# Performance work log

Hardware: AMD Instinct MI355X
Metric: run time of the kernel (lower is better)

The kernel has to match this reference:

```python
import jax, jax.numpy as jnp
import numpy as np

B, S, DIM = 4, 512, 2048
E, INTER = 32, 1024
G, TOPK_G, TOPK = 8, 4, 6
ROUTE_SCALE = 2.5
SHARED_INTER = 2 * INTER  # n_shared_experts * moe_inter_dim


def setup_inputs() -> dict:
    key = jax.random.key(0)
    ks = jax.random.split(key, 8)
    sd = 0.02
    return {
        "x": jax.random.normal(ks[0], (B, S, DIM), jnp.float32),
        "gate_w": jax.random.normal(ks[1], (E, DIM), jnp.float32) * sd,
        "w11": jax.random.normal(ks[2], (E, INTER, DIM), jnp.float32) * sd,  # gate proj (torch Linear weight [out,in])
        "w33": jax.random.normal(ks[3], (E, INTER, DIM), jnp.float32) * sd,  # up proj
        "w22": jax.random.normal(ks[4], (E, DIM, INTER), jnp.float32) * sd,  # down proj
        "sw1": jax.random.normal(ks[5], (SHARED_INTER, DIM), jnp.float32) * sd,
        "sw2": jax.random.normal(ks[6], (DIM, SHARED_INTER), jnp.float32) * sd,
        "sw3": jax.random.normal(ks[7], (SHARED_INTER, DIM), jnp.float32) * sd,
    }


def _gate(xf, gate_w):
    # sigmoid scores, group-limited greedy top-k (bias=None branch)
    scores = jax.nn.sigmoid(xf @ gate_w.T)                      # [T, E]
    gs = scores.reshape(-1, G, E // G)                          # [T, G, E/G]
    group_scores = gs.max(axis=-1)                              # amax since bias is None
    _, gidx = jax.lax.top_k(group_scores, TOPK_G)               # [T, TOPK_G]
    gmask = jnp.any(jnp.arange(G)[None, None, :] == gidx[:, :, None], axis=1)  # [T, G] keep-mask
    masked = jnp.where(gmask[:, :, None], gs, -jnp.inf).reshape(-1, E)
    _, idx = jax.lax.top_k(masked, TOPK)                        # [T, TOPK]
    w = jnp.take_along_axis(scores, idx, axis=1)                # gather from original (pre-mask) scores
    w = w / jnp.sum(w, axis=-1, keepdims=True) * ROUTE_SCALE    # sigmoid normalization + route_scale
    return w, idx


def reference(x, gate_w, w11, w33, w22, sw1, sw2, sw3):
    xf = x.reshape(-1, DIM)                                     # [T, D]
    T = xf.shape[0]
    w, idx = _gate(xf, gate_w)
    # dense combine weights: equals the gather->gmm->scatter*prob of the original
    c = jnp.zeros((T, E), xf.dtype).at[jnp.arange(T)[:, None], idx].add(w)  # [T, E]
    g = jnp.einsum('td,eid->tei', xf, w11)                      # fc1 (gate)
    u = jnp.einsum('td,eid->tei', xf, w33)                      # fc2 (up)
    act = jax.nn.silu(g) * u                                    # fused SiLU gating
    y = jnp.einsum('tei,te,edi->td', act, c, w22)               # down proj + weighted combine
    shared = (jax.nn.silu(xf @ sw1.T) * (xf @ sw3.T)) @ sw2.T   # shared experts MLP
    return (y + shared).reshape(x.shape)
```

## Files before the change

kernel.cpp:

```cpp
#include <hip/hip_runtime.h>
#include <hip/hip_bf16.h>

#define T_TOK  2048
#define DIMSZ  2048
#define NEXP   32
#define INTERS 1024
#define SINTER 2048
#define NTOPK  6

typedef __bf16 bf16x8 __attribute__((ext_vector_type(8)));
typedef float  f32x4  __attribute__((ext_vector_type(4)));
typedef unsigned short u16x8 __attribute__((ext_vector_type(8)));

__device__ __forceinline__ unsigned short f2b(float f) {
    __hip_bfloat16 h = __float2bfloat16(f);
    return __builtin_bit_cast(unsigned short, h);
}

__device__ __forceinline__ void gl_lds16(const unsigned short* g, unsigned short* l) {
    __builtin_amdgcn_global_load_lds(
        (const __attribute__((address_space(1))) void*)g,
        (__attribute__((address_space(3))) void*)l, 16, 0, 0);
}
__device__ __forceinline__ void gl_lds16f(const float* g, float* l) {
    __builtin_amdgcn_global_load_lds(
        (const __attribute__((address_space(1))) void*)g,
        (__attribute__((address_space(3))) void*)l, 16, 0, 0);
}

__device__ __forceinline__ bf16x8 cvt8(float4 lo, float4 hi) {
    u16x8 u;
    u[0] = f2b(lo.x); u[1] = f2b(lo.y); u[2] = f2b(lo.z); u[3] = f2b(lo.w);
    u[4] = f2b(hi.x); u[5] = f2b(hi.y); u[6] = f2b(hi.z); u[7] = f2b(hi.w);
    return __builtin_bit_cast(bf16x8, u);
}

__global__ void cvt_f2b(const float4* __restrict__ src, unsigned short* __restrict__ dst, int n8) {
    int stride = gridDim.x * blockDim.x;
    for (int i = blockIdx.x * blockDim.x + threadIdx.x; i < n8; i += stride) {
        float4 a = src[2 * (size_t)i];
        float4 b = src[2 * (size_t)i + 1];
        u16x8 o;
        o[0] = f2b(a.x); o[1] = f2b(a.y); o[2] = f2b(a.z); o[3] = f2b(a.w);
        o[4] = f2b(b.x); o[5] = f2b(b.y); o[6] = f2b(b.z); o[7] = f2b(b.w);
        *(u16x8*)&dst[(size_t)i * 8] = o;
    }
}

#define SCT 8
#define SCK 128
__global__ __launch_bounds__(256) void gate_scores_kernel(
    const float* __restrict__ x, const float* __restrict__ gw, float* __restrict__ scores)
{
    __shared__ float xs[SCT * SCK];
    __shared__ float gs[NEXP * (SCK + 1)];
    const int t0 = blockIdx.x * SCT;
    const int tid = threadIdx.x;
    const int tl = tid >> 5, e = tid & 31;
    float acc = 0.f;
    for (int k0 = 0; k0 < DIMSZ; k0 += SCK) {
        {
            int row = tid >> 5, d4 = tid & 31;
            *(float4*)&xs[row * SCK + d4 * 4] =
                *(const float4*)&x[(size_t)(t0 + row) * DIMSZ + k0 + d4 * 4];
        }
        #pragma unroll
        for (int i = 0; i < 4; ++i) {
            int lin = tid + i * 256;
            int row = lin >> 5, d4 = lin & 31;
            float4 v = *(const float4*)&gw[(size_t)row * DIMSZ + k0 + d4 * 4];
            float* dst = &gs[row * (SCK + 1) + d4 * 4];
            dst[0] = v.x; dst[1] = v.y; dst[2] = v.z; dst[3] = v.w;
        }
        __syncthreads();
        #pragma unroll 8
        for (int d = 0; d < SCK; ++d)
            acc += xs[tl * SCK + d] * gs[e * (SCK + 1) + d];
        __syncthreads();
    }
    scores[(size_t)(t0 + tl) * NEXP + e] = 1.f / (1.f + expf(-acc));
}

__global__ __launch_bounds__(256) void topk_kernel(
    const float* __restrict__ scores,
    int* __restrict__ counts, int* __restrict__ toklist, float* __restrict__ wgts)
{
    int t = blockIdx.x * 256 + threadIdx.x;
    if (t >= T_TOK) return;
    float sc[NEXP];
    #pragma unroll
    for (int e = 0; e < NEXP; ++e) sc[e] = scores[(size_t)t * NEXP + e];

    float gsc[8];
    #pragma unroll
    for (int g = 0; g < 8; ++g) {
        float m = sc[4 * g];
        #pragma unroll
        for (int j = 1; j < 4; ++j) m = fmaxf(m, sc[4 * g + j]);
        gsc[g] = m;
    }
    bool gsel[8] = {false, false, false, false, false, false, false, false};
    for (int it = 0; it < 4; ++it) {
        int bi = -1; float bv = -1e30f;
        #pragma unroll
        for (int g = 0; g < 8; ++g)
            if (!gsel[g] && gsc[g] > bv) { bv = gsc[g]; bi = g; }
        gsel[bi] = true;
    }
    bool esel[NEXP];
    #pragma unroll
    for (int e = 0; e < NEXP; ++e) esel[e] = false;
    int   idx[NTOPK];
    float w[NTOPK];
    float sum = 0.f;
    for (int it = 0; it < NTOPK; ++it) {
        int bi = -1; float bv = -1e30f;
        #pragma unroll
        for (int e = 0; e < NEXP; ++e) {
            if (!gsel[e >> 2] || esel[e]) continue;
            if (sc[e] > bv) { bv = sc[e]; bi = e; }
        }
        esel[bi] = true; idx[it] = bi; w[it] = bv; sum += bv;
    }
    float scale = 2.5f / sum;
    for (int k = 0; k < NTOPK; ++k) {
        int e = idx[k];
        int s = atomicAdd(&counts[e], 1);
        toklist[e * T_TOK + s] = (t << 3) | k;
        wgts[e * T_TOK + s]   = w[k] * scale;
    }
}

__device__ __forceinline__ void walk_experts(
    int ty, const int* __restrict__ counts, int& fe, int& fy, int& frb)
{
    int acc2 = 0, rb = 0;
    fe = -1; fy = 0; frb = 0;
    #pragma unroll
    for (int e2 = 0; e2 < NEXP; ++e2) {
        const int cnt = counts[e2];
        const int nt = (cnt + 127) >> 7;
        if (fe < 0 && ty < acc2 + nt) { fe = e2; fy = ty - acc2; frb = rb; }
        acc2 += nt; rb += cnt;
    }
}

__global__ __launch_bounds__(256, 3) void fc1_all(
    const unsigned short* __restrict__ A,
    const float* __restrict__ w11, const float* __restrict__ w33,
    const float* __restrict__ sw1, const float* __restrict__ sw3,
    unsigned short* __restrict__ h, unsigned short* __restrict__ hs,
    const int* __restrict__ counts, const int* __restrict__ toklist)
{
    constexpr int BK = 64, K = DIMSZ, NT = K / BK;
    __shared__ unsigned short As[128 * 64];
    __shared__ float B1s[64 * 64];
    __shared__ float B2s[64 * 64];

    const int tid = threadIdx.x;
    bool SH; int e, m0, n0, hbase = 0;
    {
        const int wgid = blockIdx.x;
        if (wgid < 512) {
            SH = true; e = NEXP; m0 = (wgid >> 5) * 128; n0 = (wgid & 31) * 64;
        } else {
            const int rid = wgid - 512;
            const int xt = rid & 15, ty = rid >> 4;
            int fe, fy, frb;
            walk_experts(ty, counts, fe, fy, frb);
            SH = false; e = fe; m0 = fy * 128; n0 = xt * 64; hbase = frb;
        }
    }
    if (!SH && e < 0) return;
    const int N = SH ? SINTER : INTERS;
    const int M = SH ? T_TOK : counts[e];

    const size_t eoff = SH ? 0 : (size_t)e * INTERS * DIMSZ;
    const float* B1 = (SH ? sw1 : w11) + eoff + (size_t)n0 * K;
    const float* B2 = (SH ? sw3 : w33) + eoff + (size_t)n0 * K;
    unsigned short* Hout = SH ? hs : h;

    const int wave = tid >> 6;
    const int lane = tid & 63;
    const int wm = (wave >> 1) * 64;
    const int wn = (wave & 1) * 32;
    const int lm = lane & 15;
    const int quad = lane >> 4;

    const unsigned short* aP[4];
    {
        const int l8 = lane >> 3;
        const int sg = (lane & 7) ^ l8;
        #pragma unroll
        for (int i = 0; i < 4; ++i) {
            const int row = (wave * 4 + i) * 8 + l8;
            const int gr = m0 + row;
            int ar;
            if (SH) ar = gr;
            else ar = (gr < M) ? (toklist[e * T_TOK + gr] >> 3) : 0;
            aP[i] = A + (size_t)ar * K + sg * 8;
        }
    }
    int offB[4];
    {
        #pragma unroll
        for (int i = 0; i < 4; ++i) {
            const int c = wave * 4 + i;
            const int row = 4 * c + (lane >> 4);
            const int g = (lane & 15) ^ (row & 7);
            offB[i] = row * K + g * 4;
        }
    }

    f32x4 acc1[4][2] = {};
    f32x4 acc2v[4][2] = {};

    for (int t = 0; t < NT; ++t) {
        const int k0 = t * BK;
        #pragma unroll
        for (int i = 0; i < 4; ++i)
            gl_lds16(aP[i] + k0, &As[(wave * 4 + i) * 512]);
        #pragma unroll
        for (int i = 0; i < 4; ++i) {
            gl_lds16f(B1 + offB[i] + k0, &B1s[(wave * 4 + i) * 256]);
            gl_lds16f(B2 + offB[i] + k0, &B2s[(wave * 4 + i) * 256]);
        }
        __syncthreads();

        #pragma unroll
        for (int kh = 0; kh < 2; ++kh) {
            const int soffA = (((kh << 2) | quad) ^ (lm & 7)) << 3;
            const int j0 = ((kh << 2) | quad) << 1;
            const int s0 = j0 ^ (lm & 7);
            const int s1 = (j0 | 1) ^ (lm & 7);
            bf16x8 af[4], bf1[2], bf2[2];
            #pragma unroll
            for (int ti = 0; ti < 4; ++ti)
                af[ti] = *(const bf16x8*)&As[(wm + ti * 16 + lm) * 64 + soffA];
            #pragma unroll
            for (int tj = 0; tj < 2; ++tj) {
                const int rB = (wn + tj * 16 + lm) * 64;
                bf1[tj] = cvt8(*(const float4*)&B1s[rB + s0 * 4],
                               *(const float4*)&B1s[rB + s1 * 4]);
                bf2[tj] = cvt8(*(const float4*)&B2s[rB + s0 * 4],
                               *(const float4*)&B2s[rB + s1 * 4]);
            }
            #pragma unroll
            for (int ti = 0; ti < 4; ++ti)
                #pragma unroll
                for (int tj = 0; tj < 2; ++tj) {
                    acc1[ti][tj] = __builtin_amdgcn_mfma_f32_16x16x32_bf16(
                        af[ti], bf1[tj], acc1[ti][tj], 0, 0, 0);
                    acc2v[ti][tj] = __builtin_amdgcn_mfma_f32_16x16x32_bf16(
                        af[ti], bf2[tj], acc2v[ti][tj], 0, 0, 0);
                }
        }
        __syncthreads();
    }

    #pragma unroll
    for (int ti = 0; ti < 4; ++ti) {
        #pragma unroll
        for (int r = 0; r < 4; ++r) {
            const int lrow = wm + ti * 16 + quad * 4 + r;
            const int grow = m0 + lrow;
            if (!SH && grow >= M) continue;
            const int cr = SH ? grow : (hbase + grow);
            #pragma unroll
            for (int tj = 0; tj < 2; ++tj) {
                int nn = n0 + wn + tj * 16 + lm;
                float g = acc1[ti][tj][r];
                float u = acc2v[ti][tj][r];
                float hv = g / (1.f + expf(-g)) * u;
                Hout[(size_t)cr * N + nn] = f2b(hv);
            }
        }
    }
}

__global__ __launch_bounds__(256, 3) void fc2_all(
    const unsigned short* __restrict__ h, const unsigned short* __restrict__ hs,
    const float* __restrict__ w22, const float* __restrict__ sw2,
    float* __restrict__ out,
    const int* __restrict__ counts, const int* __restrict__ toklist,
    const float* __restrict__ wgts)
{
    constexpr int BK = 32;
    __shared__ unsigned short As[128 * 32];
    __shared__ float Bs[128 * 32];

    const int tid = threadIdx.x;
    bool SH; int e, m0, n0, hbase = 0;
    {
        const int wgid = blockIdx.x;
        if (wgid < 256) {
            SH = true; e = NEXP; m0 = (wgid >> 4) * 128; n0 = (wgid & 15) * 128;
        } else {
            const int rid = wgid - 256;
            const int xt = rid & 15, ty = rid >> 4;
            int fe, fy, frb;
            walk_experts(ty, counts, fe, fy, frb);
            SH = false; e = fe; m0 = fy * 128; n0 = xt * 128; hbase = frb;
        }
    }
    if (!SH && e < 0) return;
    const int K = SH ? SINTER : INTERS;
    const int NT = K / BK;
    const int M = SH ? T_TOK : counts[e];
    if (m0 >= M) return;

    const unsigned short* Asrc = SH ? hs : h;
    const float* B = (SH ? sw2 : (w22 + (size_t)e * DIMSZ * INTERS)) + (size_t)n0 * K;

    const int wave = tid >> 6;
    const int lane = tid & 63;
    const int wm = (wave >> 1) * 64;
    const int wn = (wave & 1) * 64;
    const int lm = lane & 15;
    const int quad = lane >> 4;

    const unsigned short* aP[2];
    {
        const int gs = (lane & 3) ^ ((lane >> 3) & 3);
        #pragma unroll
        for (int i = 0; i < 2; ++i) {
            const int row = (wave * 2 + i) * 16 + (lane >> 2);
            const int gr = m0 + row;
            int ar;
            if (SH) ar = gr;
            else ar = hbase + ((gr < M) ? gr : 0);
            aP[i] = Asrc + (size_t)ar * K + gs * 8;
        }
    }
    int offB[4];
    {
        const int gs = (lane & 7) ^ (lane >> 3);
        #pragma unroll
        for (int i = 0; i < 4; ++i) {
            const int row = (wave * 4 + i) * 8 + (lane >> 3);
            offB[i] = row * K + gs * 4;
        }
    }

    f32x4 acc[4][4] = {};

    const int ga = quad ^ ((lm >> 1) & 3);
    const int s0 = (quad << 1) ^ (lm & 7);
    const int s1 = s0 ^ 1;

    for (int t = 0; t < NT; ++t) {
        const int k0 = t * BK;
        #pragma unroll
        for (int i = 0; i < 2; ++i)
            gl_lds16(aP[i] + k0, &As[(wave * 2 + i) * 512]);
        #pragma unroll
        for (int i = 0; i < 4; ++i)
            gl_lds16f(B + offB[i] + k0, &Bs[(wave * 4 + i) * 256]);
        __syncthreads();

        bf16x8 af[4], bfr[4];
        #pragma unroll
        for (int ti = 0; ti < 4; ++ti)
            af[ti] = *(const bf16x8*)&As[(wm + ti * 16 + lm) * 32 + ga * 8];
        #pragma unroll
        for (int tj = 0; tj < 4; ++tj) {
            const int rB = (wn + tj * 16 + lm) * 32;
            bfr[tj] = cvt8(*(const float4*)&Bs[rB + s0 * 4],
                           *(const float4*)&Bs[rB + s1 * 4]);
        }
        #pragma unroll
        for (int ti = 0; ti < 4; ++ti)
            #pragma unroll
            for (int tj = 0; tj < 4; ++tj)
                acc[ti][tj] = __builtin_amdgcn_mfma_f32_16x16x32_bf16(
                    af[ti], bfr[tj], acc[ti][tj], 0, 0, 0);

        __syncthreads();
    }

    #pragma unroll
    for (int ti = 0; ti < 4; ++ti) {
        #pragma unroll
        for (int r = 0; r < 4; ++r) {
            const int lrow = wm + ti * 16 + quad * 4 + r;
            const int grow = m0 + lrow;
            int cr; float cw;
            if (SH) { cr = grow; cw = 1.f; }
            else {
                if (grow >= M) continue;
                int ent = toklist[e * T_TOK + grow];
                cr = ent >> 3;
                cw = wgts[e * T_TOK + grow];
            }
            #pragma unroll
            for (int tj = 0; tj < 4; ++tj) {
                int nn = n0 + wn + tj * 16 + lm;
                atomicAdd(&out[(size_t)cr * DIMSZ + nn], acc[ti][tj][r] * cw);
            }
        }
    }
}

extern "C" void kernel_launch(void* const* d_in, const int* in_sizes, int n_in,
                              void* d_out, int out_size, void* d_ws, size_t ws_size,
                              hipStream_t stream)
{
    const float* x   = (const float*)d_in[0];
    const float* gw  = (const float*)d_in[1];
    const float* w11 = (const float*)d_in[2];
    const float* w33 = (const float*)d_in[3];
    const float* w22 = (const float*)d_in[4];
    const float* sw1 = (const float*)d_in[5];
    const float* sw2 = (const float*)d_in[6];
    const float* sw3 = (const float*)d_in[7];
    float* out = (float*)d_out;

    char* ws = (char*)d_ws;
    size_t off = 0;
    auto alloc = [&](size_t b) { void* p = ws + off; off = (off + b + 255) & ~(size_t)255; return p; };
    int*            counts  = (int*)alloc(NEXP * 4);
    int*            toklist = (int*)alloc((size_t)NEXP * T_TOK * 4);
    float*          wgts    = (float*)alloc((size_t)NEXP * T_TOK * 4);
    float*          scores  = (float*)alloc((size_t)T_TOK * NEXP * 4);
    unsigned short* xb      = (unsigned short*)alloc((size_t)T_TOK * DIMSZ * 2);
    unsigned short* h       = (unsigned short*)alloc(((size_t)T_TOK * NTOPK + 128) * INTERS * 2);
    unsigned short* hs      = (unsigned short*)alloc((size_t)T_TOK * SINTER * 2);

    hipMemsetAsync(counts, 0, NEXP * 4, stream);
    hipMemsetAsync(out, 0, out_size, stream);

    cvt_f2b<<<1024, 256, 0, stream>>>((const float4*)x, xb, T_TOK * DIMSZ / 8);

    gate_scores_kernel<<<T_TOK / SCT, 256, 0, stream>>>(x, gw, scores);
    topk_kernel<<<(T_TOK + 255) / 256, 256, 0, stream>>>(scores, counts, toklist, wgts);

    fc1_all<<<512 + 2048, 256, 0, stream>>>(
        xb, w11, w33, sw1, sw3, h, hs, counts, toklist);

    fc2_all<<<256 + 2048, 256, 0, stream>>>(
        h, hs, w22, sw2, out, counts, toklist, wgts);
}
```

Baseline: 1.040 ms.

## Double-buffer LDS tiles in fc1 and fc2 to overlap loads with MFMA

```diff
diff --git a/kernel.cpp b/kernel.cpp
--- a/kernel.cpp
+++ b/kernel.cpp
@@ -152,10 +152,10 @@
     unsigned short* __restrict__ h, unsigned short* __restrict__ hs,
     const int* __restrict__ counts, const int* __restrict__ toklist)
 {
-    constexpr int BK = 64, K = DIMSZ, NT = K / BK;
-    __shared__ unsigned short As[128 * 64];
-    __shared__ float B1s[64 * 64];
-    __shared__ float B2s[64 * 64];
+    constexpr int BK = 32, K = DIMSZ, NT = K / BK;
+    __shared__ unsigned short As[2][128 * 32];
+    __shared__ float B1s[2][64 * 32];
+    __shared__ float B2s[2][64 * 32];
 
     const int tid = threadIdx.x;
     bool SH; int e, m0, n0, hbase = 0;
@@ -187,75 +187,80 @@
     const int lm = lane & 15;
     const int quad = lane >> 4;
 
-    const unsigned short* aP[4];
-    {
-        const int l8 = lane >> 3;
-        const int sg = (lane & 7) ^ l8;
-        #pragma unroll
-        for (int i = 0; i < 4; ++i) {
-            const int row = (wave * 4 + i) * 8 + l8;
+    const unsigned short* aP[2];
+    {
+        const int gs = (lane & 3) ^ ((lane >> 3) & 3);
+        #pragma unroll
+        for (int i = 0; i < 2; ++i) {
+            const int row = (wave * 2 + i) * 16 + (lane >> 2);
             const int gr = m0 + row;
             int ar;
             if (SH) ar = gr;
             else ar = (gr < M) ? (toklist[e * T_TOK + gr] >> 3) : 0;
-            aP[i] = A + (size_t)ar * K + sg * 8;
-        }
-    }
-    int offB[4];
-    {
-        #pragma unroll
-        for (int i = 0; i < 4; ++i) {
-            const int c = wave * 4 + i;
-            const int row = 4 * c + (lane >> 4);
-            const int g = (lane & 15) ^ (row & 7);
-            offB[i] = row * K + g * 4;
+            aP[i] = A + (size_t)ar * K + gs * 8;
+        }
+    }
+    int offB[2];
+    {
+        const int gs = (lane & 7) ^ (lane >> 3);
+        #pragma unroll
+        for (int i = 0; i < 2; ++i) {
+            const int row = (wave * 2 + i) * 8 + (lane >> 3);
+            offB[i] = row * K + gs * 4;
         }
     }
 
     f32x4 acc1[4][2] = {};
     f32x4 acc2v[4][2] = {};
 
+    const int ga = quad ^ ((lm >> 1) & 3);
+    const int s0 = (quad << 1) ^ (lm & 7);
+    const int s1 = s0 ^ 1;
+
+    #pragma unroll
+    for (int i = 0; i < 2; ++i) {
+        gl_lds16(aP[i], &As[0][(wave * 2 + i) * 512]);
+        gl_lds16f(B1 + offB[i], &B1s[0][(wave * 2 + i) * 256]);
+        gl_lds16f(B2 + offB[i], &B2s[0][(wave * 2 + i) * 256]);
+    }
+    __syncthreads();
+
+    int buf = 0;
     for (int t = 0; t < NT; ++t) {
-        const int k0 = t * BK;
-        #pragma unroll
-        for (int i = 0; i < 4; ++i)
-            gl_lds16(aP[i] + k0, &As[(wave * 4 + i) * 512]);
-        #pragma unroll
-        for (int i = 0; i < 4; ++i) {
-            gl_lds16f(B1 + offB[i] + k0, &B1s[(wave * 4 + i) * 256]);
-            gl_lds16f(B2 + offB[i] + k0, &B2s[(wave * 4 + i) * 256]);
-        }
+        if (t + 1 < NT) {
+            const int kn = (t + 1) * BK;
+            #pragma unroll
+            for (int i = 0; i < 2; ++i) {
+                gl_lds16(aP[i] + kn, &As[buf ^ 1][(wave * 2 + i) * 512]);
+                gl_lds16f(B1 + offB[i] + kn, &B1s[buf ^ 1][(wave * 2 + i) * 256]);
+                gl_lds16f(B2 + offB[i] + kn, &B2s[buf ^ 1][(wave * 2 + i) * 256]);
+            }
+        }
+
+        bf16x8 af[4], bf1[2], bf2[2];
+        #pragma unroll
+        for (int ti = 0; ti < 4; ++ti)
+            af[ti] = *(const bf16x8*)&As[buf][(wm + ti * 16 + lm) * 32 + ga * 8];
+        #pragma unroll
+        for (int tj = 0; tj < 2; ++tj) {
+            const int rB = (wn + tj * 16 + lm) * 32;
+            bf1[tj] = cvt8(*(const float4*)&B1s[buf][rB + s0 * 4],
+                           *(const float4*)&B1s[buf][rB + s1 * 4]);
+            bf2[tj] = cvt8(*(const float4*)&B2s[buf][rB + s0 * 4],
+                           *(const float4*)&B2s[buf][rB + s1 * 4]);
+        }
+        #pragma unroll
+        for (int ti = 0; ti < 4; ++ti)
+            #pragma unroll
+            for (int tj = 0; tj < 2; ++tj) {
+                acc1[ti][tj] = __builtin_amdgcn_mfma_f32_16x16x32_bf16(
+                    af[ti], bf1[tj], acc1[ti][tj], 0, 0, 0);
+                acc2v[ti][tj] = __builtin_amdgcn_mfma_f32_16x16x32_bf16(
+                    af[ti], bf2[tj], acc2v[ti][tj], 0, 0, 0);
+            }
+
         __syncthreads();
-
-        #pragma unroll
-        for (int kh = 0; kh < 2; ++kh) {
-            const int soffA = (((kh << 2) | quad) ^ (lm & 7)) << 3;
-            const int j0 = ((kh << 2) | quad) << 1;
-            const int s0 = j0 ^ (lm & 7);
-            const int s1 = (j0 | 1) ^ (lm & 7);
-            bf16x8 af[4], bf1[2], bf2[2];
-            #pragma unroll
-            for (int ti = 0; ti < 4; ++ti)
-                af[ti] = *(const bf16x8*)&As[(wm + ti * 16 + lm) * 64 + soffA];
-            #pragma unroll
-            for (int tj = 0; tj < 2; ++tj) {
-                const int rB = (wn + tj * 16 + lm) * 64;
-                bf1[tj] = cvt8(*(const float4*)&B1s[rB + s0 * 4],
-                               *(const float4*)&B1s[rB + s1 * 4]);
-                bf2[tj] = cvt8(*(const float4*)&B2s[rB + s0 * 4],
-                               *(const float4*)&B2s[rB + s1 * 4]);
-            }
-            #pragma unroll
-            for (int ti = 0; ti < 4; ++ti)
-                #pragma unroll
-                for (int tj = 0; tj < 2; ++tj) {
-                    acc1[ti][tj] = __builtin_amdgcn_mfma_f32_16x16x32_bf16(
-                        af[ti], bf1[tj], acc1[ti][tj], 0, 0, 0);
-                    acc2v[ti][tj] = __builtin_amdgcn_mfma_f32_16x16x32_bf16(
-                        af[ti], bf2[tj], acc2v[ti][tj], 0, 0, 0);
-                }
-        }
-        __syncthreads();
+        buf ^= 1;
     }
 
     #pragma unroll
@@ -286,8 +291,8 @@
     const float* __restrict__ wgts)
 {
     constexpr int BK = 32;
-    __shared__ unsigned short As[128 * 32];
-    __shared__ float Bs[128 * 32];
+    __shared__ unsigned short As[2][128 * 32];
+    __shared__ float Bs[2][128 * 32];
 
     const int tid = threadIdx.x;
     bool SH; int e, m0, n0, hbase = 0;
@@ -348,25 +353,35 @@
     const int s0 = (quad << 1) ^ (lm & 7);
     const int s1 = s0 ^ 1;
 
+    #pragma unroll
+    for (int i = 0; i < 2; ++i)
+        gl_lds16(aP[i], &As[0][(wave * 2 + i) * 512]);
+    #pragma unroll
+    for (int i = 0; i < 4; ++i)
+        gl_lds16f(B + offB[i], &Bs[0][(wave * 4 + i) * 256]);
+    __syncthreads();
+
+    int buf = 0;
     for (int t = 0; t < NT; ++t) {
-        const int k0 = t * BK;
-        #pragma unroll
-        for (int i = 0; i < 2; ++i)
-            gl_lds16(aP[i] + k0, &As[(wave * 2 + i) * 512]);
-        #pragma unroll
-        for (int i = 0; i < 4; ++i)
-            gl_lds16f(B + offB[i] + k0, &Bs[(wave * 4 + i) * 256]);
-        __syncthreads();
+        if (t + 1 < NT) {
+            const int kn = (t + 1) * BK;
+            #pragma unroll
+            for (int i = 0; i < 2; ++i)
+                gl_lds16(aP[i] + kn, &As[buf ^ 1][(wave * 2 + i) * 512]);
+            #pragma unroll
+            for (int i = 0; i < 4; ++i)
+                gl_lds16f(B + offB[i] + kn, &Bs[buf ^ 1][(wave * 4 + i) * 256]);
+        }
 
         bf16x8 af[4], bfr[4];
         #pragma unroll
         for (int ti = 0; ti < 4; ++ti)
-            af[ti] = *(const bf16x8*)&As[(wm + ti * 16 + lm) * 32 + ga * 8];
+            af[ti] = *(const bf16x8*)&As[buf][(wm + ti * 16 + lm) * 32 + ga * 8];
         #pragma unroll
         for (int tj = 0; tj < 4; ++tj) {
             const int rB = (wn + tj * 16 + lm) * 32;
-            bfr[tj] = cvt8(*(const float4*)&Bs[rB + s0 * 4],
-                           *(const float4*)&Bs[rB + s1 * 4]);
+            bfr[tj] = cvt8(*(const float4*)&Bs[buf][rB + s0 * 4],
+                           *(const float4*)&Bs[buf][rB + s1 * 4]);
         }
         #pragma unroll
         for (int ti = 0; ti < 4; ++ti)
@@ -376,6 +391,7 @@
                     af[ti], bfr[tj], acc[ti][tj], 0, 0, 0);
 
         __syncthreads();
+        buf ^= 1;
     }
 
     #pragma unroll
```

Result: slower. 1.171 ms (+12.5%).
